# Kernel tuning notes

Measured on AMD Instinct MI355X. Metric: run time of the kernel, lower is better.

The kernel has to match this reference:

```python
import jax, jax.numpy as jnp
import numpy as np

# Model dims (from MambaLayer: Mamba2(d_model=256, d_state=128, d_conv=4, expand=2, headdim=64))
D_MODEL = 256
D_INNER = 512
D_STATE = 128
NHEADS = 8
HEADDIM = 64
D_CONV = 4
CONV_DIM = D_INNER + 2 * D_STATE          # 768
D_IN_PROJ = 2 * D_INNER + 2 * D_STATE + NHEADS  # 1288
ATT_HEADS = 8
MLP_HID = 4 * D_MODEL
NUM_CLASSES = 2


def _mamba2(x, in_proj_w, conv_w, conv_b, dt_bias, A_log, D_param, norm_w, out_proj_w):
    """Mamba2 forward (SSD selective scan), ngroups=1, no in_proj/out_proj bias."""
    b, L, _ = x.shape
    zxbcdt = x @ in_proj_w.T                                   # (b,L,1288)
    z = zxbcdt[..., :D_INNER]                                   # gate
    xBC = zxbcdt[..., D_INNER:D_INNER + CONV_DIM]
    dt = jax.nn.softplus(zxbcdt[..., -NHEADS:] + dt_bias)       # (b,L,h)
    # depthwise causal conv1d (kernel 4) + SiLU
    xpad = jnp.pad(xBC, ((0, 0), (D_CONV - 1, 0), (0, 0)))
    xBC = sum(conv_w[:, k] * xpad[:, k:k + L, :] for k in range(D_CONV)) + conv_b
    xBC = jax.nn.silu(xBC)
    xs = xBC[..., :D_INNER].reshape(b, L, NHEADS, HEADDIM)      # (b,L,h,p)
    Bm = xBC[..., D_INNER:D_INNER + D_STATE]                    # (b,L,n)
    Cm = xBC[..., D_INNER + D_STATE:]                           # (b,L,n)
    dA = jnp.exp(dt * (-jnp.exp(A_log)))                        # (b,L,h)

    def step(h_prev, inp):
        dA_t, dt_t, B_t, C_t, x_t = inp                         # (b,h),(b,h),(b,n),(b,n),(b,h,p)
        h = h_prev * dA_t[..., None, None] + (dt_t[..., None] * x_t)[..., None] * B_t[:, None, None, :]
        return h, jnp.einsum('bhpn,bn->bhp', h, C_t)

    tfirst = lambda a: jnp.moveaxis(a, 1, 0)
    h0 = jnp.zeros((b, NHEADS, HEADDIM, D_STATE), x.dtype)
    _, ys = jax.lax.scan(step, h0, (tfirst(dA), tfirst(dt), tfirst(Bm), tfirst(Cm), tfirst(xs)))
    y = jnp.moveaxis(ys, 0, 1) + D_param[None, None, :, None] * xs
    # gated RMSNorm then out projection
    y = y.reshape(b, L, D_INNER) * jax.nn.silu(z)
    y = y * jax.lax.rsqrt(jnp.mean(y * y, -1, keepdims=True) + 1e-5) * norm_w
    return y @ out_proj_w.T


def _cross_attn(x, ctx, wq, wk, wv, wo, wo_b, w1, b1, ln_w, ln_b, w2, b2):
    """CrossModalAttention.forward: attn -> out_proj -> Mlp (no residual, per source)."""
    b, t, c = x.shape
    hd = c // ATT_HEADS
    heads = lambda a: a.reshape(b, -1, ATT_HEADS, hd).transpose(0, 2, 1, 3)
    q, k, v = heads(x @ wq.T), heads(ctx @ wk.T), heads(ctx @ wv.T)
    att = jax.nn.softmax(jnp.einsum('bhxd,bhyd->bhxy', q, k) * (hd ** -0.5), axis=-1)
    o = jnp.einsum('bhxy,bhyd->bhxd', att, v).transpose(0, 2, 1, 3).reshape(b, t, c)
    o = o @ wo.T + wo_b
    h = jax.nn.gelu(o @ w1.T + b1, approximate=False)
    mu = jnp.mean(h, -1, keepdims=True)
    var = jnp.mean((h - mu) ** 2, -1, keepdims=True)
    h = (h - mu) * jax.lax.rsqrt(var + 1e-5) * ln_w + ln_b
    return h @ w2.T + b2


def setup_inputs() -> dict:
    key = jax.random.key(0)
    ks = iter(jax.random.split(key, 32))
    f32 = jnp.float32
    w = lambda *s: jax.random.normal(next(ks), s, f32) * 0.02
    return {
        'x': jax.random.normal(next(ks), (2, 2048, D_MODEL), f32),
        'context': jax.random.normal(next(ks), (2, 2048, D_MODEL), f32),
        'in_proj_w': w(D_IN_PROJ, D_MODEL),
        'conv_w': w(CONV_DIM, D_CONV),
        'conv_b': jnp.zeros((CONV_DIM,), f32),
        'dt_bias': jax.random.normal(next(ks), (NHEADS,), f32) * 0.5,
        'A_log': jnp.log(jnp.linspace(1.0, 16.0, NHEADS).astype(f32)),
        'D_param': jnp.ones((NHEADS,), f32),
        'norm_w': jnp.ones((D_INNER,), f32),
        'out_proj_w': w(D_MODEL, D_INNER),
        'wq': w(D_MODEL, D_MODEL),
        'wk': w(D_MODEL, D_MODEL),
        'wv': w(D_MODEL, D_MODEL),
        'wo': w(D_MODEL, D_MODEL),
        'wo_b': jnp.zeros((D_MODEL,), f32),
        'w1': w(MLP_HID, D_MODEL),
        'b1': jnp.zeros((MLP_HID,), f32),
        'ln_w': jnp.ones((MLP_HID,), f32),
        'ln_b': jnp.zeros((MLP_HID,), f32),
        'w2': w(D_MODEL, MLP_HID),
        'b2': jnp.zeros((D_MODEL,), f32),
        'head_w': w(NUM_CLASSES, D_MODEL),
        'head_b': jnp.zeros((NUM_CLASSES,), f32),
    }


def reference(x, context, in_proj_w, conv_w, conv_b, dt_bias, A_log, D_param, norm_w, out_proj_w,
              wq, wk, wv, wo, wo_b, w1, b1, ln_w, ln_b, w2, b2, head_w, head_b):
    h = x + _mamba2(x, in_proj_w, conv_w, conv_b, dt_bias, A_log, D_param, norm_w, out_proj_w)
    h = _cross_attn(h, context, wq, wk, wv, wo, wo_b, w1, b1, ln_w, ln_b, w2, b2)
    # ClsHead: mean-pool over tokens, linear to classes
    return jnp.mean(h, axis=1) @ head_w.T + head_b
```

## Files before the change

kernel.cpp:

```cpp
#include <hip/hip_runtime.h>
#include <hip/hip_bf16.h>
#include <math.h>

#define DEVFN __device__ __forceinline__

constexpr int BATCH = 2;
constexpr int SEQ   = 2048;
constexpr int DM    = 256;
constexpr int DI    = 512;
constexpr int DSTATE= 128;
constexpr int NH    = 8;
constexpr int HD    = 64;
constexpr int CDIM  = 768;
constexpr int DPROJ = 1288;
constexpr int MTOK  = BATCH*SEQ;
constexpr int HID   = 1024;
constexpr int CHUNK = 32;
constexpr int NCHUNK= SEQ/CHUNK;
constexpr int NSPLIT= 8;
constexpr int KVLEN = SEQ/NSPLIT;
constexpr int NKT   = KVLEN/64;

constexpr int W_INPROJ = 0;
constexpr int W_OUTPROJ= 329728;
constexpr int W_Q      = 460800;
constexpr int W_K      = 526336;
constexpr int W_V      = 591872;
constexpr int W_O      = 657408;
constexpr int W_1      = 722944;
constexpr int W_TOT    = 985088;

typedef __bf16 bf16x8 __attribute__((ext_vector_type(8)));
typedef __bf16 bf16x4 __attribute__((ext_vector_type(4)));
typedef __bf16 bf16x2 __attribute__((ext_vector_type(2)));
typedef float  f32x4  __attribute__((ext_vector_type(4)));

DEVFN float gelu_exact(float x){ return 0.5f*x*(1.f+erff(x*0.70710678118654752f)); }
DEVFN float silu_f(float x){ return x/(1.f+expf(-x)); }

DEVFN bf16x8 pack8(float4 a, float4 b){
  bf16x8 r;
  r[0]=(__bf16)a.x; r[1]=(__bf16)a.y; r[2]=(__bf16)a.z; r[3]=(__bf16)a.w;
  r[4]=(__bf16)b.x; r[5]=(__bf16)b.y; r[6]=(__bf16)b.z; r[7]=(__bf16)b.w;
  return r;
}
DEVFN f32x4 mfma16(bf16x8 a, bf16x8 b, f32x4 c){
  return __builtin_amdgcn_mfma_f32_16x16x32_bf16(a, b, c, 0, 0, 0);
}

__global__ __launch_bounds__(256)
void cvt_w(const float* __restrict__ w_inproj, const float* __restrict__ w_outproj,
           const float* __restrict__ wq, const float* __restrict__ wk,
           const float* __restrict__ wv, const float* __restrict__ wo,
           const float* __restrict__ w1, __bf16* __restrict__ wbf)
{
  int i4 = (blockIdx.x*256 + threadIdx.x)*4;
  const float* src;
  if      (i4 < W_OUTPROJ) src = w_inproj  + i4;
  else if (i4 < W_Q)       src = w_outproj + (i4 - W_OUTPROJ);
  else if (i4 < W_K)       src = wq + (i4 - W_Q);
  else if (i4 < W_V)       src = wk + (i4 - W_K);
  else if (i4 < W_O)       src = wv + (i4 - W_V);
  else if (i4 < W_1)       src = wo + (i4 - W_O);
  else                     src = w1 + (i4 - W_1);
  float4 v = *(const float4*)src;
  bf16x4 o;
  o[0]=(__bf16)v.x; o[1]=(__bf16)v.y; o[2]=(__bf16)v.z; o[3]=(__bf16)v.w;
  *(bf16x4*)(wbf + i4) = o;
}

template<int ACT, bool HASBIAS, bool AF32>
__global__ __launch_bounds__(256)
void gemm64x(const void* __restrict__ Av, const __bf16* __restrict__ W,
             const float* __restrict__ bias, __bf16* __restrict__ C,
             int M, int N, int K)
{
  __shared__ __bf16 As[64][40];
  __shared__ __bf16 Ws[64][40];
  const int tid = threadIdx.x;
  const int bm = blockIdx.x*64, bn = blockIdx.y*64;
  const int w = tid >> 6, lane = tid & 63;
  const int quad = lane >> 4, mr = lane & 15;
  const int wm = (w >> 1) * 32, wn = (w & 1) * 32;
  const int srow = tid >> 2, skc = (tid & 3) * 8;

  const float*  apf = (const float*)Av + (size_t)(bm + srow)*K + skc;
  const __bf16* apb = (const __bf16*)Av + (size_t)(bm + srow)*K + skc;
  const bool wok = (bn + srow) < N;
  const __bf16* wp = W + (size_t)(bn + srow)*K + skc;

  bf16x8 zb{};
  bf16x8 a0;
  if (AF32) a0 = pack8(*(const float4*)apf, *(const float4*)(apf+4));
  else      a0 = *(const bf16x8*)apb;
  bf16x8 w0 = wok ? *(const bf16x8*)wp : zb;

  f32x4 acc[2][2];
  #pragma unroll
  for (int i=0;i<2;i++)
    #pragma unroll
    for (int j=0;j<2;j++) acc[i][j] = f32x4{0.f,0.f,0.f,0.f};

  for (int k0 = 0; k0 < K; k0 += 32){
    __syncthreads();
    *(bf16x8*)&As[srow][skc] = a0;
    *(bf16x8*)&Ws[srow][skc] = w0;
    __syncthreads();
    if (k0 + 32 < K){
      if (AF32) a0 = pack8(*(const float4*)(apf+k0+32), *(const float4*)(apf+k0+36));
      else      a0 = *(const bf16x8*)(apb+k0+32);
      w0 = wok ? *(const bf16x8*)(wp+k0+32) : zb;
    }
    bf16x8 af[2], bfr[2];
    af[0]  = *(const bf16x8*)&As[wm      + mr][quad*8];
    af[1]  = *(const bf16x8*)&As[wm + 16 + mr][quad*8];
    bfr[0] = *(const bf16x8*)&Ws[wn      + mr][quad*8];
    bfr[1] = *(const bf16x8*)&Ws[wn + 16 + mr][quad*8];
    #pragma unroll
    for (int i=0;i<2;i++)
      #pragma unroll
      for (int j=0;j<2;j++)
        acc[i][j] = mfma16(af[i], bfr[j], acc[i][j]);
  }

  #pragma unroll
  for (int j=0;j<2;j++){
    int col = bn + wn + j*16 + mr;
    if (col >= N) continue;
    float bb = HASBIAS ? bias[col] : 0.f;
    #pragma unroll
    for (int i=0;i<2;i++)
      #pragma unroll
      for (int reg=0;reg<4;reg++){
        int row = bm + wm + i*16 + quad*4 + reg;
        float vv = acc[i][j][reg] + bb;
        if (ACT == 1) vv = gelu_exact(vv);
        C[(size_t)row*N + col] = (__bf16)vv;
      }
  }
}

template<bool HASBIAS, bool HASRESF>
__global__ __launch_bounds__(256)
void gemm64b(const __bf16* __restrict__ A, const __bf16* __restrict__ W,
             const float* __restrict__ bias, const float* __restrict__ residf,
             __bf16* __restrict__ Cb, int M, int N, int K)
{
  __shared__ __bf16 As[64][40];
  __shared__ __bf16 Ws[64][40];
  const int tid = threadIdx.x;
  const int bm = blockIdx.x*64, bn = blockIdx.y*64;
  const int w = tid >> 6, lane = tid & 63;
  const int quad = lane >> 4, mr = lane & 15;
  const int wm = (w >> 1) * 32, wn = (w & 1) * 32;
  const int srow = tid >> 2, skc = (tid & 3) * 8;

  const __bf16* ap = A + (size_t)(bm + srow)*K + skc;
  const __bf16* wp = W + (size_t)(bn + srow)*K + skc;
  bf16x8 a0 = *(const bf16x8*)ap;
  bf16x8 w0 = *(const bf16x8*)wp;

  f32x4 acc[2][2];
  #pragma unroll
  for (int i=0;i<2;i++)
    #pragma unroll
    for (int j=0;j<2;j++) acc[i][j] = f32x4{0.f,0.f,0.f,0.f};

  for (int k0 = 0; k0 < K; k0 += 32){
    __syncthreads();
    *(bf16x8*)&As[srow][skc] = a0;
    *(bf16x8*)&Ws[srow][skc] = w0;
    __syncthreads();
    if (k0 + 32 < K){
      a0 = *(const bf16x8*)(ap+k0+32);
      w0 = *(const bf16x8*)(wp+k0+32);
    }
    bf16x8 af[2], bfr[2];
    af[0]  = *(const bf16x8*)&As[wm      + mr][quad*8];
    af[1]  = *(const bf16x8*)&As[wm + 16 + mr][quad*8];
    bfr[0] = *(const bf16x8*)&Ws[wn      + mr][quad*8];
    bfr[1] = *(const bf16x8*)&Ws[wn + 16 + mr][quad*8];
    #pragma unroll
    for (int i=0;i<2;i++)
      #pragma unroll
      for (int j=0;j<2;j++)
        acc[i][j] = mfma16(af[i], bfr[j], acc[i][j]);
  }

  #pragma unroll
  for (int j=0;j<2;j++){
    int col = bn + wn + j*16 + mr;
    float bb = HASBIAS ? bias[col] : 0.f;
    #pragma unroll
    for (int i=0;i<2;i++)
      #pragma unroll
      for (int reg=0;reg<4;reg++){
        int row = bm + wm + i*16 + quad*4 + reg;
        float vv = acc[i][j][reg] + bb;
        if (HASRESF) vv += residf[(size_t)row*N + col];
        Cb[(size_t)row*N + col] = (__bf16)vv;
      }
  }
}

__global__ __launch_bounds__(256)
void qkv_gemm(const __bf16* __restrict__ hres, const float* __restrict__ ctx,
              const __bf16* __restrict__ wbf, __bf16* __restrict__ qo,
              __bf16* __restrict__ ko, __bf16* __restrict__ vt)
{
  __shared__ __bf16 As[64][40];
  __shared__ __bf16 Ws[64][40];
  const int tid = threadIdx.x;
  const int bm = blockIdx.x*64, bn = blockIdx.y*64, z = blockIdx.z;
  const int K = DM, N = DM;
  const bool abf = (z == 0);
  const __bf16* W = wbf + ((z == 0) ? W_Q : (z == 1) ? W_K : W_V);
  const int w = tid >> 6, lane = tid & 63;
  const int quad = lane >> 4, mr = lane & 15;
  const int wm = (w >> 1) * 32, wn = (w & 1) * 32;
  const int srow = tid >> 2, skc = (tid & 3) * 8;

  const __bf16* apb = hres + (size_t)(bm + srow)*K + skc;
  const float*  apf = ctx  + (size_t)(bm + srow)*K + skc;
  const __bf16* wp  = W + (size_t)(bn + srow)*K + skc;
  bf16x8 a0;
  if (abf) a0 = *(const bf16x8*)apb;
  else     a0 = pack8(*(const float4*)apf, *(const float4*)(apf+4));
  bf16x8 w0 = *(const bf16x8*)wp;

  f32x4 acc[2][2];
  #pragma unroll
  for (int i=0;i<2;i++)
    #pragma unroll
    for (int j=0;j<2;j++) acc[i][j] = f32x4{0.f,0.f,0.f,0.f};

  for (int k0 = 0; k0 < K; k0 += 32){
    __syncthreads();
    *(bf16x8*)&As[srow][skc] = a0;
    *(bf16x8*)&Ws[srow][skc] = w0;
    __syncthreads();
    if (k0 + 32 < K){
      if (abf) a0 = *(const bf16x8*)(apb+k0+32);
      else     a0 = pack8(*(const float4*)(apf+k0+32), *(const float4*)(apf+k0+36));
      w0 = *(const bf16x8*)(wp+k0+32);
    }
    bf16x8 af[2], bfr[2];
    af[0]  = *(const bf16x8*)&As[wm      + mr][quad*8];
    af[1]  = *(const bf16x8*)&As[wm + 16 + mr][quad*8];
    bfr[0] = *(const bf16x8*)&Ws[wn      + mr][quad*8];
    bfr[1] = *(const bf16x8*)&Ws[wn + 16 + mr][quad*8];
    #pragma unroll
    for (int i=0;i<2;i++)
      #pragma unroll
      for (int j=0;j<2;j++)
        acc[i][j] = mfma16(af[i], bfr[j], acc[i][j]);
  }

  if (z < 2){
    __bf16* C = (z == 0) ? qo : ko;
    #pragma unroll
    for (int j=0;j<2;j++){
      int col = bn + wn + j*16 + mr;
      #pragma unroll
      for (int i=0;i<2;i++)
        #pragma unroll
        for (int reg=0;reg<4;reg++){
          int row = bm + wm + i*16 + quad*4 + reg;
          C[(size_t)row*N + col] = (__bf16)acc[i][j][reg];
        }
    }
  } else {
    #pragma unroll
    for (int j=0;j<2;j++){
      int col = bn + wn + j*16 + mr;
      int h = col >> 5, dl = col & 31;
      #pragma unroll
      for (int i=0;i<2;i++){
        int rowb = bm + wm + i*16 + quad*4;
        int b = rowb >> 11, t = rowb & 2047;
        bf16x4 o;
        #pragma unroll
        for (int reg=0;reg<4;reg++) o[reg] = (__bf16)acc[i][j][reg];
        *(bf16x4*)(vt + ((size_t)(b*NH + h)*32 + dl)*SEQ + t) = o;
      }
    }
  }
}

__global__ __launch_bounds__(256)
void conv_dt_kernel(const __bf16* __restrict__ zx, const float* __restrict__ convw,
                    const float* __restrict__ convb, const float* __restrict__ dt_bias,
                    const float* __restrict__ A_log, __bf16* __restrict__ xBC,
                    float* __restrict__ dtb, float* __restrict__ ldab)
{
  int idx = blockIdx.x*256 + threadIdx.x;
  int c4 = (idx % (CDIM/4))*4;
  int bt = idx / (CDIM/4);
  int b = bt >> 11, t = bt & 2047;
  float acc[4];
  float4 cb = *(const float4*)(convb + c4);
  acc[0]=cb.x; acc[1]=cb.y; acc[2]=cb.z; acc[3]=cb.w;
  float4 wrow[4];
  #pragma unroll
  for (int j=0;j<4;j++) wrow[j] = *(const float4*)(convw + (c4+j)*4);
  #pragma unroll
  for (int k=0;k<4;k++){
    int ts = t - 3 + k;
    if (ts >= 0){
      bf16x4 xv = *(const bf16x4*)(zx + (size_t)(b*SEQ + ts)*DPROJ + DI + c4);
      const float* wk4[4] = {(const float*)&wrow[0], (const float*)&wrow[1],
                             (const float*)&wrow[2], (const float*)&wrow[3]};
      #pragma unroll
      for (int j=0;j<4;j++) acc[j] = fmaf(wk4[j][k], (float)xv[j], acc[j]);
    }
  }
  bf16x4 o;
  #pragma unroll
  for (int j=0;j<4;j++) o[j] = (__bf16)silu_f(acc[j]);
  *(bf16x4*)(xBC + (size_t)bt*CDIM + c4) = o;
  if (c4 < NH){
    #pragma unroll
    for (int j=0;j<4;j++){
      int h = c4 + j;
      float raw = (float)zx[(size_t)bt*DPROJ + 2*DI + 2*DSTATE + h] + dt_bias[h];
      float dt = fmaxf(raw, 0.f) + log1pf(expf(-fabsf(raw)));
      int oo = (b*NH + h)*SEQ + t;
      dtb[oo]  = dt;
      ldab[oo] = -__expf(A_log[h]) * dt;
    }
  }
}

__global__ __launch_bounds__(256)
void chunk_state(const __bf16* __restrict__ xBC, const float* __restrict__ dtb,
                 const float* __restrict__ ldab, __bf16* __restrict__ Hc,
                 float* __restrict__ Ac)
{
  const int blk = blockIdx.x;
  const int ch = blk & 63, bh = blk >> 6;
  const int b = bh >> 3, h = bh & 7;
  const int t0 = ch*CHUNK;
  const int tid = threadIdx.x;
  __shared__ float csS[CHUNK], wendS[CHUNK];
  __shared__ __bf16 Xw[64][40];
  __shared__ __bf16 Bt[128][40];

  if (tid < 32){
    float v  = ldab[bh*SEQ + t0 + tid];
    float dtv = dtb[bh*SEQ + t0 + tid];
    #pragma unroll
    for (int off=1; off<32; off<<=1){
      float o = __shfl_up(v, off, 32);
      if (tid >= off) v += o;
    }
    csS[tid] = v;
    float cs31 = __shfl(v, 31, 32);
    wendS[tid] = __expf(cs31 - v) * dtv;
  }
  __syncthreads();
  {
    int s  = tid >> 3;
    int pg = (tid & 7) * 8;
    bf16x8 xv = *(const bf16x8*)(xBC + (size_t)(b*SEQ + t0 + s)*CDIM + h*HD + pg);
    float wgt = wendS[s];
    #pragma unroll
    for (int e=0;e<8;e++) Xw[pg+e][s] = (__bf16)((float)xv[e] * wgt);
    int ng = (tid & 7) * 16;
    const __bf16* bp = xBC + (size_t)(b*SEQ + t0 + s)*CDIM + DI + ng;
    bf16x8 b0 = *(const bf16x8*)bp;
    bf16x8 b1 = *(const bf16x8*)(bp+8);
    #pragma unroll
    for (int e=0;e<8;e++){ Bt[ng+e][s] = b0[e]; Bt[ng+8+e][s] = b1[e]; }
  }
  if (tid == 0) Ac[blk] = __expf(csS[31]);
  __syncthreads();

  const int w = tid >> 6, lane = tid & 63, quad = lane >> 4, mr = lane & 15;
  bf16x8 af = *(const bf16x8*)&Xw[w*16 + mr][quad*8];
  __bf16* out = Hc + (size_t)blk*8192;
  #pragma unroll
  for (int j=0;j<8;j++){
    bf16x8 bfm = *(const bf16x8*)&Bt[j*16 + mr][quad*8];
    f32x4 a = mfma16(af, bfm, f32x4{0.f,0.f,0.f,0.f});
    #pragma unroll
    for (int reg=0; reg<4; reg++){
      int p = w*16 + quad*4 + reg;
      out[p*128 + j*16 + mr] = (__bf16)a[reg];
    }
  }
}

__global__ __launch_bounds__(256)
void state_prefix(__bf16* __restrict__ Hc, const float* __restrict__ Ac)
{
  const int blk = blockIdx.x;
  const int bh = blk >> 4, sub = blk & 15;
  const int tid = threadIdx.x;
  const int off = sub*512 + tid*2;
  __shared__ float AcS[64];
  if (tid < 64) AcS[tid] = Ac[bh*64 + tid];
  __bf16* base = Hc + (size_t)bh*64*8192 + off;
  bf16x2 v[64];
  #pragma unroll
  for (int c=0;c<64;c++) v[c] = *(const bf16x2*)(base + (size_t)c*8192);
  __syncthreads();
  float r0 = 0.f, r1 = 0.f;
  #pragma unroll
  for (int c=0;c<64;c++){
    bf16x2 o; o[0] = (__bf16)r0; o[1] = (__bf16)r1;
    *(bf16x2*)(base + (size_t)c*8192) = o;
    float a = AcS[c];
    r0 = fmaf(a, r0, (float)v[c][0]);
    r1 = fmaf(a, r1, (float)v[c][1]);
  }
}

__global__ __launch_bounds__(256)
void chunk_out(const __bf16* __restrict__ xBC, const float* __restrict__ dtb,
               const float* __restrict__ ldab, const __bf16* __restrict__ h0buf,
               const float* __restrict__ Dparam, __bf16* __restrict__ ybuf)
{
  const int blk = blockIdx.x;
  const int ch = blk & 63, bh = blk >> 6;
  const int b = bh >> 3, h = bh & 7;
  const int t0 = ch*CHUNK;
  const int tid = threadIdx.x;
  __shared__ float csS[CHUNK], dtS[CHUNK];
  __shared__ __bf16 Xct[64][40];
  __shared__ __bf16 Ms[32][40];

  if (tid < 32){
    float v = ldab[bh*SEQ + t0 + tid];
    dtS[tid] = dtb[bh*SEQ + t0 + tid];
    #pragma unroll
    for (int off=1; off<32; off<<=1){
      float o = __shfl_up(v, off, 32);
      if (tid >= off) v += o;
    }
    csS[tid] = v;
  }
  __syncthreads();
  {
    int s  = tid >> 3;
    int pg = (tid & 7) * 8;
    bf16x8 xv = *(const bf16x8*)(xBC + (size_t)(b*SEQ + t0 + s)*CDIM + h*HD + pg);
    #pragma unroll
    for (int e=0;e<8;e++) Xct[pg+e][s] = xv[e];
  }

  const int w = tid >> 6, lane = tid & 63, quad = lane >> 4, mr = lane & 15;
  const int ti = w >> 1, si = w & 1;

  const __bf16* Crow = xBC + (size_t)(b*SEQ + t0 + ti*16 + mr)*CDIM + DI + DSTATE;
  bf16x8 af[4];
  #pragma unroll
  for (int kk=0; kk<4; kk++)
    af[kk] = *(const bf16x8*)(Crow + kk*32 + quad*8);
  f32x4 sacc = f32x4{0.f,0.f,0.f,0.f};
  const __bf16* Brow = xBC + (size_t)(b*SEQ + t0 + si*16 + mr)*CDIM + DI;
  #pragma unroll
  for (int kk=0; kk<4; kk++){
    bf16x8 bfm = *(const bf16x8*)(Brow + kk*32 + quad*8);
    sacc = mfma16(af[kk], bfm, sacc);
  }
  #pragma unroll
  for (int reg=0; reg<4; reg++){
    int t = ti*16 + quad*4 + reg;
    int s = si*16 + mr;
    float m = 0.f;
    if (s <= t) m = __expf(csS[t] - csS[s]) * dtS[s] * sacc[reg];
    Ms[t][s] = (__bf16)m;
  }
  __syncthreads();

  f32x4 acc[2] = { f32x4{0.f,0.f,0.f,0.f}, f32x4{0.f,0.f,0.f,0.f} };
  const __bf16* h0r = h0buf + (size_t)blk*8192;
  #pragma unroll
  for (int j=0;j<2;j++){
    int p = (si*2 + j)*16 + mr;
    #pragma unroll
    for (int kk=0; kk<4; kk++){
      bf16x8 bh0 = *(const bf16x8*)(h0r + (size_t)p*128 + kk*32 + quad*8);
      acc[j] = mfma16(af[kk], bh0, acc[j]);
    }
  }
  #pragma unroll
  for (int reg=0;reg<4;reg++){
    int t = ti*16 + quad*4 + reg;
    float e = __expf(csS[t]);
    acc[0][reg] *= e;
    acc[1][reg] *= e;
  }
  bf16x8 am = *(const bf16x8*)&Ms[ti*16 + mr][quad*8];
  #pragma unroll
  for (int j=0;j<2;j++){
    int p = (si*2 + j)*16 + mr;
    bf16x8 bx = *(const bf16x8*)&Xct[p][quad*8];
    acc[j] = mfma16(am, bx, acc[j]);
  }
  const float Dv = Dparam[h];
  #pragma unroll
  for (int j=0;j<2;j++){
    int p = (si*2 + j)*16 + mr;
    #pragma unroll
    for (int reg=0;reg<4;reg++){
      int t = t0 + ti*16 + quad*4 + reg;
      float xv = (float)xBC[(size_t)(b*SEQ + t)*CDIM + h*HD + p];
      ybuf[(size_t)(b*SEQ + t)*DI + h*HD + p] = (__bf16)fmaf(Dv, xv, acc[j][reg]);
    }
  }
}

__global__ __launch_bounds__(128)
void rmsgate_kernel(__bf16* __restrict__ y, const __bf16* __restrict__ zx,
                    const float* __restrict__ normw)
{
  const int row = blockIdx.x, tid = threadIdx.x;
  const __bf16* zrow = zx + (size_t)row*DPROJ;
  __bf16* yrow = y + (size_t)row*DI;
  bf16x4 yv = *(const bf16x4*)(yrow + tid*4);
  bf16x4 zv = *(const bf16x4*)(zrow + tid*4);
  float g[4];
  float ss = 0.f;
  #pragma unroll
  for (int e=0;e<4;e++){
    g[e] = (float)yv[e] * silu_f((float)zv[e]);
    ss += g[e]*g[e];
  }
  #pragma unroll
  for (int off=1; off<64; off<<=1) ss += __shfl_xor(ss, off);
  __shared__ float red[2];
  if ((tid & 63)==0) red[tid>>6] = ss;
  __syncthreads();
  float tot = red[0] + red[1];
  float rs = rsqrtf(tot * (1.f/DI) + 1e-5f);
  float4 nw = *(const float4*)(normw + tid*4);
  const float* nwp = (const float*)&nw;
  bf16x4 o;
  #pragma unroll
  for (int e=0;e<4;e++) o[e] = (__bf16)(g[e]*rs*nwp[e]);
  *(bf16x4*)(yrow + tid*4) = o;
}

__global__ __launch_bounds__(256)
void flash_part(const __bf16* __restrict__ qb, const __bf16* __restrict__ kb,
                const __bf16* __restrict__ vt, float* __restrict__ opart,
                float* __restrict__ lpart)
{
  const int qt = blockIdx.x, ksp = blockIdx.y, bh = blockIdx.z;
  const int b = bh >> 3, h = bh & 7;
  const int tid = threadIdx.x;
  const int w = tid >> 6, lane = tid & 63;
  const int quad = lane >> 4, mr = lane & 15;
  const int qrow0 = b*SEQ + qt*128 + w*32;
  const float SC = 0.17677669529663687f;
  __shared__ __bf16 Pq[4][32][72];

  const __bf16* kbase_p = kb + (size_t)(b*SEQ + ksp*KVLEN + mr)*DM + h*32 + quad*8;
  const __bf16* vbase_p = vt + ((size_t)bh*32 + mr)*SEQ + ksp*KVLEN + quad*8;

  bf16x8 bq[2];
  #pragma unroll
  for (int i2=0;i2<2;i2++)
    bq[i2] = *(const bf16x8*)(qb + (size_t)(qrow0 + i2*16 + mr)*DM + h*32 + quad*8);

  f32x4 accO[2][2];
  #pragma unroll
  for (int i=0;i<2;i++)
    #pragma unroll
    for (int j=0;j<2;j++) accO[i][j] = f32x4{0.f,0.f,0.f,0.f};
  float lacc[2] = {0.f, 0.f};

  bf16x8 akc[4], bvc[2][2];
  #pragma unroll
  for (int ik=0;ik<4;ik++)
    akc[ik] = *(const bf16x8*)(kbase_p + (size_t)ik*16*DM);
  #pragma unroll
  for (int ks=0;ks<2;ks++)
    #pragma unroll
    for (int j2=0;j2<2;j2++)
      bvc[ks][j2] = *(const bf16x8*)(vbase_p + (size_t)j2*16*SEQ + ks*32);

  for (int kt=0; kt<NKT; kt++){
    bf16x8 akn[4], bvn[2][2];
    if (kt + 1 < NKT){
      #pragma unroll
      for (int ik=0;ik<4;ik++)
        akn[ik] = *(const bf16x8*)(kbase_p + (size_t)(kt+1)*64*DM + (size_t)ik*16*DM);
      #pragma unroll
      for (int ks=0;ks<2;ks++)
        #pragma unroll
        for (int j2=0;j2<2;j2++)
          bvn[ks][j2] = *(const bf16x8*)(vbase_p + (size_t)j2*16*SEQ + (kt+1)*64 + ks*32);
    }
    #pragma unroll
    for (int ik=0; ik<4; ik++){
      #pragma unroll
      for (int jq=0; jq<2; jq++){
        f32x4 st = mfma16(akc[ik], bq[jq], f32x4{0.f,0.f,0.f,0.f});
        bf16x4 e4;
        #pragma unroll
        for (int reg=0; reg<4; reg++){
          float e = __expf(st[reg] * SC);
          lacc[jq] += e;
          e4[reg] = (__bf16)e;
        }
        *(bf16x4*)&Pq[w][jq*16 + mr][ik*16 + quad*4] = e4;
      }
    }
    #pragma unroll
    for (int ks=0; ks<2; ks++){
      bf16x8 pa0 = *(const bf16x8*)&Pq[w][     mr][ks*32 + quad*8];
      bf16x8 pa1 = *(const bf16x8*)&Pq[w][16 + mr][ks*32 + quad*8];
      #pragma unroll
      for (int j2=0; j2<2; j2++){
        accO[0][j2] = mfma16(pa0, bvc[ks][j2], accO[0][j2]);
        accO[1][j2] = mfma16(pa1, bvc[ks][j2], accO[1][j2]);
      }
    }
    #pragma unroll
    for (int ik=0;ik<4;ik++) akc[ik] = akn[ik];
    #pragma unroll
    for (int ks=0;ks<2;ks++)
      #pragma unroll
      for (int j2=0;j2<2;j2++) bvc[ks][j2] = bvn[ks][j2];
  }

  #pragma unroll
  for (int jq=0;jq<2;jq++){
    float v = lacc[jq];
    v += __shfl_xor(v, 16);
    v += __shfl_xor(v, 32);
    lacc[jq] = v;
  }
  #pragma unroll
  for (int i2=0;i2<2;i2++)
    #pragma unroll
    for (int j2=0;j2<2;j2++)
      #pragma unroll
      for (int reg=0;reg<4;reg++){
        int row = qrow0 + i2*16 + quad*4 + reg;
        opart[((size_t)ksp*MTOK + row)*DM + h*32 + j2*16 + mr] = accO[i2][j2][reg];
      }
  if (quad == 0){
    #pragma unroll
    for (int jq=0;jq<2;jq++)
      lpart[((size_t)ksp*16 + bh)*SEQ + (qt*128 + w*32 + jq*16 + mr)] = lacc[jq];
  }
}

__global__ __launch_bounds__(256)
void flash_combine(const float* __restrict__ opart, const float* __restrict__ lpart,
                   __bf16* __restrict__ o)
{
  int idx = blockIdx.x*256 + threadIdx.x;
  int row = idx >> 6, d4 = (idx & 63)*4;
  int h = d4 >> 5;
  int b = row >> 11, t = row & 2047;
  float sx=0.f, sy=0.f, sz=0.f, sw=0.f, lsum=0.f;
  #pragma unroll
  for (int s4=0; s4<NSPLIT; s4++){
    float4 vv = *(const float4*)(opart + ((size_t)s4*MTOK + row)*DM + d4);
    sx += vv.x; sy += vv.y; sz += vv.z; sw += vv.w;
    lsum += lpart[((size_t)s4*16 + b*8 + h)*SEQ + t];
  }
  float inv = 1.f / lsum;
  bf16x4 ov;
  ov[0]=(__bf16)(sx*inv); ov[1]=(__bf16)(sy*inv);
  ov[2]=(__bf16)(sz*inv); ov[3]=(__bf16)(sw*inv);
  *(bf16x4*)(o + (size_t)row*DM + d4) = ov;
}

__global__ __launch_bounds__(256)
void ln_pool(const __bf16* __restrict__ h1, const float* __restrict__ lnw,
             const float* __restrict__ lnb, float* __restrict__ pp)
{
  const int blk = blockIdx.x;
  const int tid = threadIdx.x;
  const int row0 = blk*16;
  __shared__ float s1[4], s2[4];
  float4 wv = *(const float4*)(lnw + tid*4);
  float4 bv = *(const float4*)(lnb + tid*4);
  const float* wp = (const float*)&wv;
  const float* bp = (const float*)&bv;
  float acc[4] = {0.f,0.f,0.f,0.f};
  for (int r=0;r<16;r++){
    bf16x4 v4 = *(const bf16x4*)(h1 + (size_t)(row0+r)*HID + tid*4);
    float v[4];
    float sum=0.f, sq=0.f;
    #pragma unroll
    for (int e=0;e<4;e++){ v[e]=(float)v4[e]; sum+=v[e]; sq+=v[e]*v[e]; }
    #pragma unroll
    for (int off=1; off<64; off<<=1){ sum += __shfl_xor(sum,off); sq += __shfl_xor(sq,off); }
    int w = tid>>6;
    __syncthreads();
    if ((tid & 63)==0){ s1[w]=sum; s2[w]=sq; }
    __syncthreads();
    sum = (s1[0]+s1[1])+(s1[2]+s1[3]);
    sq  = (s2[0]+s2[1])+(s2[2]+s2[3]);
    float mu = sum * (1.f/HID);
    float var = sq * (1.f/HID) - mu*mu;
    float rstd = rsqrtf(var + 1e-5f);
    #pragma unroll
    for (int e=0;e<4;e++) acc[e] += (v[e]-mu)*rstd*wp[e] + bp[e];
  }
  *(float4*)(pp + (size_t)blk*HID + tid*4) = make_float4(acc[0],acc[1],acc[2],acc[3]);
}

__global__ __launch_bounds__(128)
void reduce_pool(const float* __restrict__ pp, float* __restrict__ pooled)
{
  const int b = blockIdx.y, cg = blockIdx.x;
  const int c = cg*128 + threadIdx.x;
  float s = 0.f;
  #pragma unroll 8
  for (int seg=0; seg<128; seg++)
    s += pp[((size_t)(b*128+seg))*HID + c];
  pooled[b*HID + c] = s * (1.f/(float)SEQ);
}

__global__ __launch_bounds__(256)
void fc2head(const float* __restrict__ pooled, const float* __restrict__ w2,
             const float* __restrict__ b2, float* __restrict__ w2h)
{
  const int b = blockIdx.y, og = blockIdx.x;
  const int tid = threadIdx.x;
  const int r = tid >> 5, l32 = tid & 31;
  const int col = og*8 + r;
  const float* wr = w2 + (size_t)col*HID + l32*32;
  const float* pv = pooled + b*HID + l32*32;
  float acc = 0.f;
  #pragma unroll
  for (int k=0;k<32;k+=4){
    float4 wv4 = *(const float4*)(wr+k);
    float4 p4  = *(const float4*)(pv+k);
    acc += wv4.x*p4.x + wv4.y*p4.y + wv4.z*p4.z + wv4.w*p4.w;
  }
  #pragma unroll
  for (int off=1; off<32; off<<=1) acc += __shfl_xor(acc, off);
  if (l32 == 0) w2h[b*DM + col] = acc + b2[col];
}

__global__ __launch_bounds__(128)
void head_final(const float* __restrict__ w2h, const float* __restrict__ hw,
                const float* __restrict__ hb, float* __restrict__ out)
{
  const int b = blockIdx.x, tid = threadIdx.x;
  int cls = tid >> 6, lane = tid & 63;
  float acc = 0.f;
  for (int c=lane;c<DM;c+=64) acc += w2h[b*DM + c]*hw[cls*DM+c];
  #pragma unroll
  for (int off=1;off<64;off<<=1) acc += __shfl_xor(acc, off);
  if (lane == 0) out[b*2 + cls] = acc + hb[cls];
}

extern "C" void kernel_launch(void* const* d_in, const int* in_sizes, int n_in,
                              void* d_out, int out_size, void* d_ws, size_t ws_size,
                              hipStream_t stream)
{
  const float* x         = (const float*)d_in[0];
  const float* context   = (const float*)d_in[1];
  const float* in_proj_w = (const float*)d_in[2];
  const float* conv_w    = (const float*)d_in[3];
  const float* conv_b    = (const float*)d_in[4];
  const float* dt_bias   = (const float*)d_in[5];
  const float* A_log     = (const float*)d_in[6];
  const float* D_param   = (const float*)d_in[7];
  const float* norm_w    = (const float*)d_in[8];
  const float* out_proj_w= (const float*)d_in[9];
  const float* wq  = (const float*)d_in[10];
  const float* wk  = (const float*)d_in[11];
  const float* wv  = (const float*)d_in[12];
  const float* wo  = (const float*)d_in[13];
  const float* wo_b= (const float*)d_in[14];
  const float* w1  = (const float*)d_in[15];
  const float* b1  = (const float*)d_in[16];
  const float* ln_w= (const float*)d_in[17];
  const float* ln_b= (const float*)d_in[18];
  const float* w2  = (const float*)d_in[19];
  const float* b2  = (const float*)d_in[20];
  const float* head_w = (const float*)d_in[21];
  const float* head_b = (const float*)d_in[22];
  float* out = (float*)d_out;
  float* ws  = (float*)d_ws;

  __bf16* zx    = (__bf16*)ws;
  __bf16* xBC   = (__bf16*)(ws + 2637824);
  float* dtb    = ws + 4210688;
  float* ldab   = ws + 4243456;
  __bf16* Hcb   = (__bf16*)(ws + 4276224);
  float* Acb    = ws + 8470528;
  __bf16* ybuf  = (__bf16*)(ws + 8471552);
  __bf16* hres  = (__bf16*)(ws + 9520128);
  __bf16* qbf   = (__bf16*)(ws + 10044416);
  __bf16* kbf   = (__bf16*)(ws + 10568704);
  __bf16* vtbf  = (__bf16*)(ws + 11092992);
  float* opart  = ws + 11617280;
  float* lpart  = ws + 20005888;
  __bf16* obf   = (__bf16*)(ws + 20268032);
  __bf16* o2bf  = (__bf16*)(ws + 20792320);
  __bf16* wbf   = (__bf16*)(ws + 21316608);
  float* pooled = ws + 21809152;
  float* w2h    = ws + 21811200;
  __bf16* h1bf  = (__bf16*)(ws + 4276224);
  float* poolp  = ws + 11617280;

  const dim3 g64(MTOK/64, DM/64);

  cvt_w<<<dim3(W_TOT/1024), dim3(256), 0, stream>>>(
      in_proj_w, out_proj_w, wq, wk, wv, wo, w1, wbf);
  gemm64x<0,false,true><<<dim3(MTOK/64, (DPROJ+63)/64), dim3(256), 0, stream>>>(
      x, wbf + W_INPROJ, nullptr, zx, MTOK, DPROJ, DM);
  conv_dt_kernel<<<dim3(MTOK*CDIM/1024), dim3(256), 0, stream>>>(
      zx, conv_w, conv_b, dt_bias, A_log, xBC, dtb, ldab);
  chunk_state<<<dim3(BATCH*NH*NCHUNK), dim3(256), 0, stream>>>(
      xBC, dtb, ldab, Hcb, Acb);
  state_prefix<<<dim3(256), dim3(256), 0, stream>>>(Hcb, Acb);
  chunk_out<<<dim3(BATCH*NH*NCHUNK), dim3(256), 0, stream>>>(
      xBC, dtb, ldab, Hcb, D_param, ybuf);
  rmsgate_kernel<<<dim3(MTOK), dim3(128), 0, stream>>>(ybuf, zx, norm_w);
  gemm64b<false,true><<<g64, dim3(256), 0, stream>>>(
      ybuf, wbf + W_OUTPROJ, nullptr, x, hres, MTOK, DM, DI);
  qkv_gemm<<<dim3(MTOK/64, DM/64, 3), dim3(256), 0, stream>>>(
      hres, context, wbf, qbf, kbf, vtbf);
  flash_part<<<dim3(SEQ/128, NSPLIT, BATCH*NH), dim3(256), 0, stream>>>(
      qbf, kbf, vtbf, opart, lpart);
  flash_combine<<<dim3(MTOK*64/256), dim3(256), 0, stream>>>(opart, lpart, obf);
  gemm64b<true,false><<<g64, dim3(256), 0, stream>>>(
      obf, wbf + W_O, wo_b, nullptr, o2bf, MTOK, DM, DM);
  gemm64x<1,true,false><<<dim3(MTOK/64, HID/64), dim3(256), 0, stream>>>(
      o2bf, wbf + W_1, b1, h1bf, MTOK, HID, DM);
  ln_pool<<<dim3(256), dim3(256), 0, stream>>>(h1bf, ln_w, ln_b, poolp);
  reduce_pool<<<dim3(8, BATCH), dim3(128), 0, stream>>>(poolp, pooled);
  fc2head<<<dim3(32, BATCH), dim3(256), 0, stream>>>(pooled, w2, b2, w2h);
  head_final<<<dim3(BATCH), dim3(128), 0, stream>>>(w2h, head_w, head_b, out);
  (void)in_sizes; (void)n_in; (void)out_size; (void)ws_size;
}
```

Before: 261.1 us.

## Store flash partials in bf16 and use one wave per row in ln_pool

The split-KV flash kernel now writes its unnormalized partial outputs as bf16 instead of fp32, and the combine kernel reads bf16. This halves the traffic of the partial buffer at some cost in precision. ln_pool is restructured so each wavefront handles whole rows with shuffle-only reductions, dropping the block-level __syncthreads and running twice as many blocks. In exchange it emits eight times as many partial pooling rows, so the small, lightly parallel reduce_pool kernel must serially sum 1024 segments per column instead of 128.

```diff
diff --git a/kernel.cpp b/kernel.cpp
--- a/kernel.cpp
+++ b/kernel.cpp
@@ -544,7 +544,7 @@
 
 __global__ __launch_bounds__(256)
 void flash_part(const __bf16* __restrict__ qb, const __bf16* __restrict__ kb,
-                const __bf16* __restrict__ vt, float* __restrict__ opart,
+                const __bf16* __restrict__ vt, __bf16* __restrict__ opart,
                 float* __restrict__ lpart)
 {
   const int qt = blockIdx.x, ksp = blockIdx.y, bh = blockIdx.z;
@@ -640,7 +640,8 @@
       #pragma unroll
       for (int reg=0;reg<4;reg++){
         int row = qrow0 + i2*16 + quad*4 + reg;
-        opart[((size_t)ksp*MTOK + row)*DM + h*32 + j2*16 + mr] = accO[i2][j2][reg];
+        opart[((size_t)ksp*MTOK + row)*DM + h*32 + j2*16 + mr]
+            = (__bf16)accO[i2][j2][reg];
       }
   if (quad == 0){
     #pragma unroll
@@ -650,24 +651,24 @@
 }
 
 __global__ __launch_bounds__(256)
-void flash_combine(const float* __restrict__ opart, const float* __restrict__ lpart,
+void flash_combine(const __bf16* __restrict__ opart, const float* __restrict__ lpart,
                    __bf16* __restrict__ o)
 {
   int idx = blockIdx.x*256 + threadIdx.x;
   int row = idx >> 6, d4 = (idx & 63)*4;
   int h = d4 >> 5;
   int b = row >> 11, t = row & 2047;
-  float sx=0.f, sy=0.f, sz=0.f, sw=0.f, lsum=0.f;
+  float s0=0.f, s1=0.f, s2=0.f, s3=0.f, lsum=0.f;
   #pragma unroll
   for (int s4=0; s4<NSPLIT; s4++){
-    float4 vv = *(const float4*)(opart + ((size_t)s4*MTOK + row)*DM + d4);
-    sx += vv.x; sy += vv.y; sz += vv.z; sw += vv.w;
+    bf16x4 vv = *(const bf16x4*)(opart + ((size_t)s4*MTOK + row)*DM + d4);
+    s0 += (float)vv[0]; s1 += (float)vv[1]; s2 += (float)vv[2]; s3 += (float)vv[3];
     lsum += lpart[((size_t)s4*16 + b*8 + h)*SEQ + t];
   }
   float inv = 1.f / lsum;
   bf16x4 ov;
-  ov[0]=(__bf16)(sx*inv); ov[1]=(__bf16)(sy*inv);
-  ov[2]=(__bf16)(sz*inv); ov[3]=(__bf16)(sw*inv);
+  ov[0]=(__bf16)(s0*inv); ov[1]=(__bf16)(s1*inv);
+  ov[2]=(__bf16)(s2*inv); ov[3]=(__bf16)(s3*inv);
   *(bf16x4*)(o + (size_t)row*DM + d4) = ov;
 }
 
@@ -677,34 +678,57 @@
 {
   const int blk = blockIdx.x;
   const int tid = threadIdx.x;
-  const int row0 = blk*16;
-  __shared__ float s1[4], s2[4];
-  float4 wv = *(const float4*)(lnw + tid*4);
-  float4 bv = *(const float4*)(lnb + tid*4);
-  const float* wp = (const float*)&wv;
-  const float* bp = (const float*)&bv;
-  float acc[4] = {0.f,0.f,0.f,0.f};
-  for (int r=0;r<16;r++){
-    bf16x4 v4 = *(const bf16x4*)(h1 + (size_t)(row0+r)*HID + tid*4);
-    float v[4];
+  const int w = tid >> 6, lane = tid & 63;
+  float4 wv[4], bv[4];
+  #pragma unroll
+  for (int c=0;c<4;c++){
+    wv[c] = *(const float4*)(lnw + c*256 + lane*4);
+    bv[c] = *(const float4*)(lnb + c*256 + lane*4);
+  }
+  float acc[4][4];
+  #pragma unroll
+  for (int c=0;c<4;c++)
+    #pragma unroll
+    for (int e=0;e<4;e++) acc[c][e]=0.f;
+
+  #pragma unroll
+  for (int r=0;r<2;r++){
+    int row = blk*8 + w*2 + r;
+    const __bf16* hr = h1 + (size_t)row*HID;
+    float v[4][4];
     float sum=0.f, sq=0.f;
     #pragma unroll
-    for (int e=0;e<4;e++){ v[e]=(float)v4[e]; sum+=v[e]; sq+=v[e]*v[e]; }
-    #pragma unroll
-    for (int off=1; off<64; off<<=1){ sum += __shfl_xor(sum,off); sq += __shfl_xor(sq,off); }
-    int w = tid>>6;
-    __syncthreads();
-    if ((tid & 63)==0){ s1[w]=sum; s2[w]=sq; }
-    __syncthreads();
-    sum = (s1[0]+s1[1])+(s1[2]+s1[3]);
-    sq  = (s2[0]+s2[1])+(s2[2]+s2[3]);
+    for (int c=0;c<4;c++){
+      bf16x4 x4 = *(const bf16x4*)(hr + c*256 + lane*4);
+      #pragma unroll
+      for (int e=0;e<4;e++){
+        v[c][e] = (float)x4[e];
+        sum += v[c][e];
+        sq  += v[c][e]*v[c][e];
+      }
+    }
+    #pragma unroll
+    for (int off=1; off<64; off<<=1){
+      sum += __shfl_xor(sum, off);
+      sq  += __shfl_xor(sq, off);
+    }
     float mu = sum * (1.f/HID);
     float var = sq * (1.f/HID) - mu*mu;
     float rstd = rsqrtf(var + 1e-5f);
     #pragma unroll
-    for (int e=0;e<4;e++) acc[e] += (v[e]-mu)*rstd*wp[e] + bp[e];
-  }
-  *(float4*)(pp + (size_t)blk*HID + tid*4) = make_float4(acc[0],acc[1],acc[2],acc[3]);
+    for (int c=0;c<4;c++){
+      const float* wp = (const float*)&wv[c];
+      const float* bp = (const float*)&bv[c];
+      #pragma unroll
+      for (int e=0;e<4;e++)
+        acc[c][e] += (v[c][e]-mu)*rstd*wp[e] + bp[e];
+    }
+  }
+  const int slot = blk*4 + w;
+  #pragma unroll
+  for (int c=0;c<4;c++)
+    *(float4*)(pp + (size_t)slot*HID + c*256 + lane*4)
+        = make_float4(acc[c][0], acc[c][1], acc[c][2], acc[c][3]);
 }
 
 __global__ __launch_bounds__(128)
@@ -714,8 +738,8 @@
   const int c = cg*128 + threadIdx.x;
   float s = 0.f;
   #pragma unroll 8
-  for (int seg=0; seg<128; seg++)
-    s += pp[((size_t)(b*128+seg))*HID + c];
+  for (int seg=0; seg<1024; seg++)
+    s += pp[((size_t)(b*1024+seg))*HID + c];
   pooled[b*HID + c] = s * (1.f/(float)SEQ);
 }
 
@@ -795,7 +819,7 @@
   __bf16* qbf   = (__bf16*)(ws + 10044416);
   __bf16* kbf   = (__bf16*)(ws + 10568704);
   __bf16* vtbf  = (__bf16*)(ws + 11092992);
-  float* opart  = ws + 11617280;
+  __bf16* opartb= (__bf16*)(ws + 11617280);
   float* lpart  = ws + 20005888;
   __bf16* obf   = (__bf16*)(ws + 20268032);
   __bf16* o2bf  = (__bf16*)(ws + 20792320);
@@ -824,13 +848,13 @@
   qkv_gemm<<<dim3(MTOK/64, DM/64, 3), dim3(256), 0, stream>>>(
       hres, context, wbf, qbf, kbf, vtbf);
   flash_part<<<dim3(SEQ/128, NSPLIT, BATCH*NH), dim3(256), 0, stream>>>(
-      qbf, kbf, vtbf, opart, lpart);
-  flash_combine<<<dim3(MTOK*64/256), dim3(256), 0, stream>>>(opart, lpart, obf);
+      qbf, kbf, vtbf, opartb, lpart);
+  flash_combine<<<dim3(MTOK*64/256), dim3(256), 0, stream>>>(opartb, lpart, obf);
   gemm64b<true,false><<<g64, dim3(256), 0, stream>>>(
       obf, wbf + W_O, wo_b, nullptr, o2bf, MTOK, DM, DM);
   gemm64x<1,true,false><<<dim3(MTOK/64, HID/64), dim3(256), 0, stream>>>(
       o2bf, wbf + W_1, b1, h1bf, MTOK, HID, DM);
-  ln_pool<<<dim3(256), dim3(256), 0, stream>>>(h1bf, ln_w, ln_b, poolp);
+  ln_pool<<<dim3(512), dim3(256), 0, stream>>>(h1bf, ln_w, ln_b, poolp);
   reduce_pool<<<dim3(8, BATCH), dim3(128), 0, stream>>>(poolp, pooled);
   fc2head<<<dim3(32, BATCH), dim3(256), 0, stream>>>(pooled, w2, b2, w2h);
   head_final<<<dim3(BATCH), dim3(128), 0, stream>>>(w2h, head_w, head_b, out);
```

Result: slower. 293.5 us (+12.4%).
